# Kernel optimization log

Hardware: AMD Instinct MI355X
Metric: run time of the kernel (lower is better)

Reference implementation:

```python
import jax, jax.numpy as jnp
import numpy as np

N, DIN, D, K0, NC = 32768, 768, 512, 128, 2
KS = [128, 64, 32, 16]  # prototype counts per stage (num_protos // 2**i)
NEG_SLOPE = 0.01


def _lin(x, W, b):
    # torch nn.Linear: W is [out, in]
    return x @ W.T + b


def _ln(x, g, b):
    m = x.mean(-1, keepdims=True)
    v = ((x - m) ** 2).mean(-1, keepdims=True)
    return (x - m) * jax.lax.rsqrt(v + 1e-5) * g + b


def setup_inputs() -> dict:
    key = jax.random.key(0)
    ks = jax.random.split(key, 40)
    s = 0.02

    def nrm(k, shp, sc=s):
        return jax.random.normal(k, shp, jnp.float32) * sc

    inp = {}
    inp["data"] = jax.random.normal(ks[0], (N, DIN), jnp.float32)
    inp["prototypes"] = jax.random.normal(ks[1], (K0, DIN), jnp.float32)
    inp["W_pp"] = nrm(ks[2], (D, DIN)); inp["b_pp"] = jnp.zeros((D,), jnp.float32)
    inp["W_cp"] = nrm(ks[3], (D, DIN)); inp["b_cp"] = jnp.zeros((D,), jnp.float32)
    inp["sim_scale"] = jnp.ones((1,), jnp.float32)
    # 3 enhancer MLPs + layernorms (stacked, same shapes)
    inp["enh_w1"] = nrm(ks[4], (3, D, D)); inp["enh_b1"] = jnp.zeros((3, D), jnp.float32)
    inp["enh_w2"] = nrm(ks[5], (3, D, D)); inp["enh_b2"] = jnp.zeros((3, D), jnp.float32)
    inp["ln_g"] = jnp.ones((3, D), jnp.float32); inp["ln_b"] = jnp.zeros((3, D), jnp.float32)
    # ProtoReducers: Mlp along K axis; fc1 [inK,inK], fc2 [outK,inK]
    ki = 6
    for i in range(3):
        inK, outK = KS[i], KS[i + 1]
        inp[f"red_w1_{i}"] = nrm(ks[ki], (inK, inK)); ki += 1
        inp[f"red_b1_{i}"] = jnp.zeros((inK,), jnp.float32)
        inp[f"red_w2_{i}"] = nrm(ks[ki], (outK, inK)); ki += 1
        inp[f"red_b2_{i}"] = jnp.zeros((outK,), jnp.float32)
    inp["W_proc"] = nrm(ks[20], (D, D)); inp["b_proc"] = jnp.zeros((D,), jnp.float32)
    inp["g_an"] = jnp.ones((D,), jnp.float32); inp["b_an"] = jnp.zeros((D,), jnp.float32)
    inp["W_t"] = nrm(ks[21], (D, D)); inp["b_t"] = jnp.zeros((D,), jnp.float32)
    inp["W_g"] = nrm(ks[22], (D, D)); inp["b_g"] = jnp.zeros((D,), jnp.float32)
    inp["W_s"] = nrm(ks[23], (1, D)); inp["b_s"] = jnp.zeros((1,), jnp.float32)
    inp["W_h"] = nrm(ks[24], (D, D)); inp["b_h"] = jnp.zeros((D,), jnp.float32)
    inp["W_c"] = nrm(ks[25], (NC, D)); inp["b_c"] = jnp.zeros((NC,), jnp.float32)
    return inp


def reference(data, prototypes, W_pp, b_pp, W_cp, b_cp, sim_scale,
              enh_w1, enh_b1, enh_w2, enh_b2, ln_g, ln_b,
              red_w1_0, red_b1_0, red_w2_0, red_b2_0,
              red_w1_1, red_b1_1, red_w2_1, red_b2_1,
              red_w1_2, red_b1_2, red_w2_2, red_b2_2,
              W_proc, b_proc, g_an, b_an,
              W_t, b_t, W_g, b_g, W_s, b_s, W_h, b_h, W_c, b_c):
    # patch / prototype projections (Linear + LeakyReLU)
    P = jax.nn.leaky_relu(_lin(data, W_pp, b_pp), NEG_SLOPE)        # [N, D]
    C = jax.nn.leaky_relu(_lin(prototypes, W_cp, b_cp), NEG_SLOPE)  # [K0, D]
    # denom = max(1e-6, tau * similarity_scale.item()); tau=1, no grad through scale
    denom = jnp.maximum(1e-6, jax.lax.stop_gradient(sim_scale)[0])
    reds = [(red_w1_0, red_b1_0, red_w2_0, red_b2_0),
            (red_w1_1, red_b1_1, red_w2_1, red_b2_1),
            (red_w1_2, red_b1_2, red_w2_2, red_b2_2)]
    for i in range(3):
        # L2 similarity: -cdist(P, C) computed as a GEMM
        d2 = (jnp.sum(P * P, -1, keepdims=True) + jnp.sum(C * C, -1)[None, :]
              - 2.0 * (P @ C.T))
        sim = -jnp.sqrt(jnp.maximum(d2, 1e-12))                     # [N, K]
        A = jax.nn.softmax(sim / denom, axis=1)                     # soft routing
        ctx = A @ C                                                 # [N, D]
        P = _ln(P + ctx, ln_g[i], ln_b[i])
        P = P + _lin(jax.nn.relu(_lin(P, enh_w1[i], enh_b1[i])), enh_w2[i], enh_b2[i])
        # ProtoReducer: Mlp over K axis (operate on C.T of shape [D, K])
        w1, b1, w2, b2 = reds[i]
        Ct = _lin(jax.nn.relu(_lin(C.T, w1, b1)), w2, b2)           # [D, Kout]
        C = Ct.T
    Z = jnp.concatenate([P, C], axis=0)                             # [N+16, D]
    Z = jax.nn.relu(_lin(Z, W_proc, b_proc))
    Z = _ln(Z, g_an, b_an)
    # gated attention MIL pooling
    t = jnp.tanh(_lin(Z, W_t, b_t))
    g = jax.nn.sigmoid(_lin(Z, W_g, b_g))
    scores = _lin(t * g, W_s, b_s)                                  # [N+16, 1]
    Aw = jax.nn.softmax(scores, axis=0)
    bag = Aw.T @ Z                                                  # [1, D]
    h = jax.nn.relu(_lin(bag, W_h, b_h))
    logits = _lin(h, W_c, b_c)                                      # [1, 2]
    return logits
```

## Files before the change

### kernel.cpp

```cpp
#include <hip/hip_runtime.h>
#include <math.h>

typedef _Float16 f16x8 __attribute__((ext_vector_type(8)));
typedef _Float16 f16x4 __attribute__((ext_vector_type(4)));
typedef float f32x4 __attribute__((ext_vector_type(4)));

#define TBM 256
#define TBN 128
#define TBK 32

#define AS1 __attribute__((address_space(1)))
#define AS3 __attribute__((address_space(3)))

__device__ __forceinline__ void gll16(const _Float16* g, _Float16* l)
{
    __builtin_amdgcn_global_load_lds((const AS1 unsigned int*)g,
                                     (AS3 unsigned int*)l, 16, 0, 0);
}

__device__ __forceinline__ int xcd_swz(int d, int nwg)
{
    int q = nwg >> 3, r = nwg & 7;
    int x = d & 7, idx = d >> 3;
    int base = x < r ? x * (q + 1) : r * (q + 1) + (x - r) * q;
    return base + idx;
}

__device__ __forceinline__ float fsigmoid(float x)
{
    return __builtin_amdgcn_rcpf(1.f + __expf(-x));
}
__device__ __forceinline__ float ftanh(float x)
{
    float ax = fabsf(x);
    float e = __expf(-2.f * ax);
    float t = (1.f - e) * __builtin_amdgcn_rcpf(1.f + e);
    return copysignf(t, x);
}

struct CvtSegs {
    const float* src[6];
    _Float16* dst[6];
    int cum4[7];
};

__global__ __launch_bounds__(256)
void cvtall_k(CvtSegs a)
{
    int total = a.cum4[6];
    for (int i = blockIdx.x * 256 + threadIdx.x; i < total; i += gridDim.x * 256) {
        int s = 0;
        while (i >= a.cum4[s + 1]) s++;
        int loc = (i - a.cum4[s]) * 4;
        float4 v = *(const float4*)(a.src[s] + loc);
        f16x4 h = { (_Float16)v.x, (_Float16)v.y, (_Float16)v.z, (_Float16)v.w };
        *(f16x4*)(a.dst[s] + loc) = h;
    }
}

template<int ACT, bool F16OUT>
__global__ __launch_bounds__(256)
void dot_k(const float* __restrict__ X, const float* __restrict__ W,
           const float* __restrict__ bias, void* __restrict__ Yv,
           int M, int K)
{
    int gw = (blockIdx.x * 256 + threadIdx.x) >> 6;
    int lane = threadIdx.x & 63;
    if (gw >= M * 512) return;
    int r = gw >> 9, n = gw & 511;
    const float* xr = X + (size_t)r * K;
    const float* wr = W + (size_t)n * K;
    float d = 0.f;
    for (int t = 0; t < K; t += 256) {
        float4 a = *(const float4*)(xr + t + lane * 4);
        float4 b = *(const float4*)(wr + t + lane * 4);
        d += a.x * b.x + a.y * b.y + a.z * b.z + a.w * b.w;
    }
#pragma unroll
    for (int o = 32; o; o >>= 1) d += __shfl_xor(d, o);
    if (lane == 0) {
        float v = d + bias[n];
        if (ACT == 1) v = v > 0.f ? v : 0.01f * v;
        else if (ACT == 2) v = fmaxf(v, 0.f);
        if (F16OUT) ((_Float16*)Yv)[(size_t)r * 512 + n] = (_Float16)v;
        else        ((float*)Yv)[(size_t)r * 512 + n] = v;
    }
}

__global__ __launch_bounds__(256)
void cvtC2_k(const float* __restrict__ C, _Float16* __restrict__ Ch,
             _Float16* __restrict__ CTh, float* __restrict__ Csq2, int Kin)
{
    int w = threadIdx.x >> 6, lane = threadIdx.x & 63;
    int row = blockIdx.x * 4 + w;
    if (row >= Kin) return;
    float4 a = *(const float4*)(C + (size_t)row * 512 + lane * 8);
    float4 b = *(const float4*)(C + (size_t)row * 512 + lane * 8 + 4);
    f16x8 h;
    h[0] = (_Float16)a.x; h[1] = (_Float16)a.y; h[2] = (_Float16)a.z; h[3] = (_Float16)a.w;
    h[4] = (_Float16)b.x; h[5] = (_Float16)b.y; h[6] = (_Float16)b.z; h[7] = (_Float16)b.w;
    *(f16x8*)(Ch + (size_t)row * 512 + lane * 8) = h;
    float s = 0.f;
#pragma unroll
    for (int q = 0; q < 8; q++) {
        float f = (float)h[q];
        s += f * f;
        CTh[(size_t)(lane * 8 + q) * Kin + row] = h[q];
    }
#pragma unroll
    for (int o = 32; o; o >>= 1) s += __shfl_xor(s, o);
    if (lane == 0) { Csq2[row * 2] = s; Csq2[row * 2 + 1] = 0.f; }
}

template<int MODE, int ACT, bool SQ>
__global__ __launch_bounds__(512)
void mgemm(const _Float16* __restrict__ A, const _Float16* __restrict__ B,
           const float* __restrict__ bias, _Float16* __restrict__ Yh,
           float* __restrict__ Psq4, int M, int K, int Nout)
{
    __shared__ _Float16 As[2][TBM * TBK];
    __shared__ _Float16 Bs[2][TBN * TBK];
    const int tid = threadIdx.x;
    const int lane = tid & 63;
    const int wid = tid >> 6;
    const int wr = wid >> 1, wc = wid & 1;

    int bid = xcd_swz(blockIdx.y * gridDim.x + blockIdx.x, gridDim.x * gridDim.y);
    const int m0 = (bid / gridDim.x) * TBM;
    const int n0 = (bid % gridDim.x) * TBN;

    f32x4 acc[4][4] = {};
    const int nt = K / TBK;

    const int lrow = lane >> 2;
    const int lk = (lane & 3) * 8;

    auto stage = [&](int t, int buf) {
        const int k0 = t * TBK;
#pragma unroll
        for (int q = 0; q < 2; q++) {
            int c = wid * 2 + q;
            int r = c * 16 + lrow;
            int am = min(m0 + r, M - 1);
            gll16(A + (size_t)am * K + k0 + lk, &As[buf][c * 512]);
        }
        {
            int c = wid;
            int r = c * 16 + lrow;
            int bn = min(n0 + r, Nout - 1);
            gll16(B + (size_t)bn * K + k0 + lk, &Bs[buf][c * 512]);
        }
    };

    stage(0, 0);
    __syncthreads();
    for (int t = 0; t < nt; ++t) {
        const int cur = t & 1;
        if (t + 1 < nt) stage(t + 1, cur ^ 1);
        f16x8 af[4], bf[4];
#pragma unroll
        for (int mi = 0; mi < 4; mi++)
            af[mi] = *(const f16x8*)(&As[cur][(wr * 64 + mi * 16 + (lane & 15)) * TBK + (lane >> 4) * 8]);
#pragma unroll
        for (int nj = 0; nj < 4; nj++)
            bf[nj] = *(const f16x8*)(&Bs[cur][(wc * 64 + nj * 16 + (lane & 15)) * TBK + (lane >> 4) * 8]);
#pragma unroll
        for (int mi = 0; mi < 4; mi++)
#pragma unroll
            for (int nj = 0; nj < 4; nj++)
                acc[mi][nj] = __builtin_amdgcn_mfma_f32_16x16x32_f16(af[mi], bf[nj], acc[mi][nj], 0, 0, 0);
        __syncthreads();
    }

    _Float16* eb = &As[0][0];
    const int g = lane >> 4;
#pragma unroll
    for (int p = 0; p < 2; p++) {
        if (p) __syncthreads();
        if ((wr >> 1) == p) {
#pragma unroll
            for (int nj = 0; nj < 4; nj++) {
                int col = wc * 64 + nj * 16 + (lane & 15);
                float bv = bias ? bias[n0 + col] : 0.f;
#pragma unroll
                for (int mi = 0; mi < 4; mi++)
#pragma unroll
                    for (int r = 0; r < 4; r++) {
                        int lr = (wr & 1) * 64 + mi * 16 + g * 4 + r;
                        float v = acc[mi][nj][r] + bv;
                        if (MODE == 0) {
                            if (ACT == 1) v = v > 0.f ? v : 0.01f * v;
                            else if (ACT == 2) v = fmaxf(v, 0.f);
                        }
                        eb[lr * 128 + col] = (_Float16)v;
                    }
            }
        }
        __syncthreads();
        int t4 = tid * 4;
        int lr = t4 >> 4;
        int cbase = (t4 & 15) * 8;
        int m = m0 + p * 128 + lr;
        float sq = 0.f;
        if (m < M) {
#pragma unroll
            for (int q = 0; q < 4; q++) {
                int c0 = cbase + q * 8;
                f16x8 hv = *(f16x8*)(eb + lr * 128 + c0);
                size_t gidx = (size_t)m * Nout + n0 + c0;
                if (MODE == 1) {
                    f16x8 old = *(f16x8*)(Yh + gidx);
                    f16x8 nw;
#pragma unroll
                    for (int e = 0; e < 8; e++) {
                        float s = (float)old[e] + (float)hv[e];
                        nw[e] = (_Float16)s;
                    }
                    *(f16x8*)(Yh + gidx) = nw;
                    hv = nw;
                } else {
                    *(f16x8*)(Yh + gidx) = hv;
                }
                if (SQ) {
#pragma unroll
                    for (int e = 0; e < 8; e++) { float f = (float)hv[e]; sq += f * f; }
                }
            }
        }
        if (SQ) {
            sq += __shfl_xor(sq, 1);
            sq += __shfl_xor(sq, 2);
            if ((lane & 3) == 0 && m < M) Psq4[(size_t)m * 4 + (n0 >> 7)] = sq;
        }
    }
}

__global__ __launch_bounds__(512)
void pgemm32(const float* __restrict__ A32, const _Float16* __restrict__ B,
             const float* __restrict__ bias, _Float16* __restrict__ Yh,
             float* __restrict__ Psq4, int M, int K, int Nout)
{
    __shared__ _Float16 As[2][TBM * TBK];
    __shared__ _Float16 Bs[2][TBN * TBK];
    const int tid = threadIdx.x;
    const int lane = tid & 63;
    const int wid = tid >> 6;
    const int wr = wid >> 1, wc = wid & 1;

    int bid = xcd_swz(blockIdx.y * gridDim.x + blockIdx.x, gridDim.x * gridDim.y);
    const int m0 = (bid / gridDim.x) * TBM;
    const int n0 = (bid % gridDim.x) * TBN;

    f32x4 acc[4][4] = {};
    const int nt = K / TBK;

    const int lrow = lane >> 2;
    const int lk = (lane & 3) * 8;

    auto stage = [&](int t, int buf) {
        const int k0 = t * TBK;
#pragma unroll
        for (int q = 0; q < 2; q++) {
            int c = wid * 2 + q;
            int r = c * 16 + lrow;
            int am = min(m0 + r, M - 1);
            const float* src = A32 + (size_t)am * K + k0 + lk;
            float4 a0 = *(const float4*)src;
            float4 a1 = *(const float4*)(src + 4);
            f16x8 h;
            h[0] = (_Float16)a0.x; h[1] = (_Float16)a0.y; h[2] = (_Float16)a0.z; h[3] = (_Float16)a0.w;
            h[4] = (_Float16)a1.x; h[5] = (_Float16)a1.y; h[6] = (_Float16)a1.z; h[7] = (_Float16)a1.w;
            *(f16x8*)(&As[buf][c * 512 + lane * 8]) = h;
        }
        {
            int c = wid;
            int r = c * 16 + lrow;
            int bn = min(n0 + r, Nout - 1);
            gll16(B + (size_t)bn * K + k0 + lk, &Bs[buf][c * 512]);
        }
    };

    stage(0, 0);
    __syncthreads();
    for (int t = 0; t < nt; ++t) {
        const int cur = t & 1;
        if (t + 1 < nt) stage(t + 1, cur ^ 1);
        f16x8 af[4], bf[4];
#pragma unroll
        for (int mi = 0; mi < 4; mi++)
            af[mi] = *(const f16x8*)(&As[cur][(wr * 64 + mi * 16 + (lane & 15)) * TBK + (lane >> 4) * 8]);
#pragma unroll
        for (int nj = 0; nj < 4; nj++)
            bf[nj] = *(const f16x8*)(&Bs[cur][(wc * 64 + nj * 16 + (lane & 15)) * TBK + (lane >> 4) * 8]);
#pragma unroll
        for (int mi = 0; mi < 4; mi++)
#pragma unroll
            for (int nj = 0; nj < 4; nj++)
                acc[mi][nj] = __builtin_amdgcn_mfma_f32_16x16x32_f16(af[mi], bf[nj], acc[mi][nj], 0, 0, 0);
        __syncthreads();
    }

    _Float16* eb = &As[0][0];
    const int g = lane >> 4;
#pragma unroll
    for (int p = 0; p < 2; p++) {
        if (p) __syncthreads();
        if ((wr >> 1) == p) {
#pragma unroll
            for (int nj = 0; nj < 4; nj++) {
                int col = wc * 64 + nj * 16 + (lane & 15);
                float bv = bias[n0 + col];
#pragma unroll
                for (int mi = 0; mi < 4; mi++)
#pragma unroll
                    for (int r = 0; r < 4; r++) {
                        int lr = (wr & 1) * 64 + mi * 16 + g * 4 + r;
                        float v = acc[mi][nj][r] + bv;
                        v = v > 0.f ? v : 0.01f * v;
                        eb[lr * 128 + col] = (_Float16)v;
                    }
            }
        }
        __syncthreads();
        int t4 = tid * 4;
        int lr = t4 >> 4;
        int cbase = (t4 & 15) * 8;
        int m = m0 + p * 128 + lr;
        float sq = 0.f;
        if (m < M) {
#pragma unroll
            for (int q = 0; q < 4; q++) {
                int c0 = cbase + q * 8;
                f16x8 hv = *(f16x8*)(eb + lr * 128 + c0);
                *(f16x8*)(Yh + (size_t)m * Nout + n0 + c0) = hv;
#pragma unroll
                for (int e = 0; e < 8; e++) { float f = (float)hv[e]; sq += f * f; }
            }
        }
        sq += __shfl_xor(sq, 1);
        sq += __shfl_xor(sq, 2);
        if ((lane & 3) == 0 && m < M) Psq4[(size_t)m * 4 + (n0 >> 7)] = sq;
    }
}

__global__ __launch_bounds__(512)
void ctxln_k(const _Float16* __restrict__ A, const _Float16* __restrict__ CT,
             const float* __restrict__ g, const float* __restrict__ b,
             _Float16* __restrict__ Ph, int M, int Kin)
{
    __shared__ _Float16 As[2][128 * TBK];
    __shared__ _Float16 Bs[2][512 * TBK];
    const int tid = threadIdx.x;
    const int lane = tid & 63;
    const int wid = tid >> 6;
    const int wr = wid >> 2, wc = wid & 3;
    const int m0 = blockIdx.y * 128;

    f32x4 acc[4][8] = {};
    const int nt = Kin / TBK;

    const int lrow = lane >> 2;
    const int lk = (lane & 3) * 8;

    auto stage = [&](int t, int buf) {
        const int k0 = t * TBK;
        {
            int r = wid * 16 + lrow;
            gll16(A + (size_t)(m0 + r) * Kin + k0 + lk, &As[buf][wid * 512]);
        }
#pragma unroll
        for (int q = 0; q < 4; q++) {
            int c = wid * 4 + q;
            int n = c * 16 + lrow;
            gll16(CT + (size_t)n * Kin + k0 + lk, &Bs[buf][c * 512]);
        }
    };

    stage(0, 0);
    __syncthreads();
    for (int t = 0; t < nt; ++t) {
        const int cur = t & 1;
        if (t + 1 < nt) stage(t + 1, cur ^ 1);
        f16x8 af[4], bf[8];
#pragma unroll
        for (int mi = 0; mi < 4; mi++)
            af[mi] = *(const f16x8*)(&As[cur][(wr * 64 + mi * 16 + (lane & 15)) * TBK + (lane >> 4) * 8]);
#pragma unroll
        for (int nj = 0; nj < 8; nj++)
            bf[nj] = *(const f16x8*)(&Bs[cur][(wc * 128 + nj * 16 + (lane & 15)) * TBK + (lane >> 4) * 8]);
#pragma unroll
        for (int mi = 0; mi < 4; mi++)
#pragma unroll
            for (int nj = 0; nj < 8; nj++)
                acc[mi][nj] = __builtin_amdgcn_mfma_f32_16x16x32_f16(af[mi], bf[nj], acc[mi][nj], 0, 0, 0);
        __syncthreads();
    }

    _Float16* eb = &Bs[0][0];
    const int gq = lane >> 4;
#pragma unroll
    for (int p = 0; p < 2; p++) {
        if (p) __syncthreads();
        if (wr == p) {
#pragma unroll
            for (int nj = 0; nj < 8; nj++) {
                int col = wc * 128 + nj * 16 + (lane & 15);
#pragma unroll
                for (int mi = 0; mi < 4; mi++)
#pragma unroll
                    for (int r = 0; r < 4; r++) {
                        int lr = mi * 16 + gq * 4 + r;
                        eb[lr * 512 + col] = (_Float16)acc[mi][nj][r];
                    }
            }
        }
        __syncthreads();
#pragma unroll
        for (int rr = 0; rr < 8; rr++) {
            int lr = wid * 8 + rr;
            int m = m0 + p * 64 + lr;
            f16x8 cv = *(f16x8*)(eb + lr * 512 + lane * 8);
            f16x8 pv = *(const f16x8*)(Ph + (size_t)m * 512 + lane * 8);
            float v[8];
            float s = 0.f, ss = 0.f;
#pragma unroll
            for (int q = 0; q < 8; q++) {
                v[q] = (float)pv[q] + (float)cv[q];
                s += v[q]; ss += v[q] * v[q];
            }
#pragma unroll
            for (int o = 32; o; o >>= 1) { s += __shfl_xor(s, o); ss += __shfl_xor(ss, o); }
            float mean = s * (1.f / 512.f);
            float var = ss * (1.f / 512.f) - mean * mean;
            float inv = 1.f / sqrtf(var + 1e-5f);
            int d0 = lane * 8;
            f16x8 o8;
#pragma unroll
            for (int q = 0; q < 8; q++)
                o8[q] = (_Float16)((v[q] - mean) * inv * g[d0 + q] + b[d0 + q]);
            *(f16x8*)(Ph + (size_t)m * 512 + d0) = o8;
        }
    }
}

__global__ __launch_bounds__(512)
void procln_k(const _Float16* __restrict__ A, const _Float16* __restrict__ W,
              const float* __restrict__ bias, const float* __restrict__ g,
              const float* __restrict__ b, _Float16* __restrict__ Zh, int M)
{
    __shared__ _Float16 As[2][128 * TBK];
    __shared__ _Float16 Bs[2][512 * TBK];
    const int tid = threadIdx.x;
    const int lane = tid & 63;
    const int wid = tid >> 6;
    const int wr = wid >> 2, wc = wid & 3;
    const int m0 = blockIdx.y * 128;
    const int K = 512;

    f32x4 acc[4][8] = {};
    const int nt = K / TBK;

    const int lrow = lane >> 2;
    const int lk = (lane & 3) * 8;

    auto stage = [&](int t, int buf) {
        const int k0 = t * TBK;
        {
            int r = wid * 16 + lrow;
            gll16(A + (size_t)(m0 + r) * K + k0 + lk, &As[buf][wid * 512]);
        }
#pragma unroll
        for (int q = 0; q < 4; q++) {
            int c = wid * 4 + q;
            int n = c * 16 + lrow;
            gll16(W + (size_t)n * K + k0 + lk, &Bs[buf][c * 512]);
        }
    };

    stage(0, 0);
    __syncthreads();
    for (int t = 0; t < nt; ++t) {
        const int cur = t & 1;
        if (t + 1 < nt) stage(t + 1, cur ^ 1);
        f16x8 af[4], bf[8];
#pragma unroll
        for (int mi = 0; mi < 4; mi++)
            af[mi] = *(const f16x8*)(&As[cur][(wr * 64 + mi * 16 + (lane & 15)) * TBK + (lane >> 4) * 8]);
#pragma unroll
        for (int nj = 0; nj < 8; nj++)
            bf[nj] = *(const f16x8*)(&Bs[cur][(wc * 128 + nj * 16 + (lane & 15)) * TBK + (lane >> 4) * 8]);
#pragma unroll
        for (int mi = 0; mi < 4; mi++)
#pragma unroll
            for (int nj = 0; nj < 8; nj++)
                acc[mi][nj] = __builtin_amdgcn_mfma_f32_16x16x32_f16(af[mi], bf[nj], acc[mi][nj], 0, 0, 0);
        __syncthreads();
    }

    _Float16* eb = &Bs[0][0];
    const int gq = lane >> 4;
#pragma unroll
    for (int p = 0; p < 2; p++) {
        if (p) __syncthreads();
        if (wr == p) {
#pragma unroll
            for (int nj = 0; nj < 8; nj++) {
                int col = wc * 128 + nj * 16 + (lane & 15);
                float bv = bias[col];
#pragma unroll
                for (int mi = 0; mi < 4; mi++)
#pragma unroll
                    for (int r = 0; r < 4; r++) {
                        int lr = mi * 16 + gq * 4 + r;
                        eb[lr * 512 + col] = (_Float16)fmaxf(acc[mi][nj][r] + bv, 0.f);
                    }
            }
        }
        __syncthreads();
#pragma unroll
        for (int rr = 0; rr < 8; rr++) {
            int lr = wid * 8 + rr;
            int m = m0 + p * 64 + lr;
            f16x8 cv = *(f16x8*)(eb + lr * 512 + lane * 8);
            float v[8];
            float s = 0.f, ss = 0.f;
#pragma unroll
            for (int q = 0; q < 8; q++) {
                v[q] = (float)cv[q];
                s += v[q]; ss += v[q] * v[q];
            }
#pragma unroll
            for (int o = 32; o; o >>= 1) { s += __shfl_xor(s, o); ss += __shfl_xor(ss, o); }
            float mean = s * (1.f / 512.f);
            float var = ss * (1.f / 512.f) - mean * mean;
            float inv = 1.f / sqrtf(var + 1e-5f);
            int d0 = lane * 8;
            f16x8 o8;
#pragma unroll
            for (int q = 0; q < 8; q++)
                o8[q] = (_Float16)((v[q] - mean) * inv * g[d0 + q] + b[d0 + q]);
            *(f16x8*)(Zh + (size_t)m * 512 + d0) = o8;
        }
    }
}

__global__ __launch_bounds__(512)
void gatgemm(const _Float16* __restrict__ A, const _Float16* __restrict__ B1,
             const _Float16* __restrict__ B2, const float* __restrict__ c1,
             const float* __restrict__ c2, const float* __restrict__ Ws,
             float* __restrict__ scr4, int M, int K, int Nout)
{
    __shared__ _Float16 As[2][TBM * TBK];
    __shared__ _Float16 B1s[2][TBN * TBK];
    __shared__ _Float16 B2s[2][TBN * TBK];
    const int tid = threadIdx.x;
    const int lane = tid & 63;
    const int wid = tid >> 6;
    const int wr = wid >> 1, wc = wid & 1;

    int bid = xcd_swz(blockIdx.y * gridDim.x + blockIdx.x, gridDim.x * gridDim.y);
    const int m0 = (bid / gridDim.x) * TBM;
    const int n0 = (bid % gridDim.x) * TBN;

    f32x4 acc1[4][4] = {};
    f32x4 acc2[4][4] = {};
    const int nt = K / TBK;

    const int lrow = lane >> 2;
    const int lk = (lane & 3) * 8;

    auto stage = [&](int t, int buf) {
        const int k0 = t * TBK;
#pragma unroll
        for (int q = 0; q < 2; q++) {
            int c = wid * 2 + q;
            int r = c * 16 + lrow;
            int am = min(m0 + r, M - 1);
            gll16(A + (size_t)am * K + k0 + lk, &As[buf][c * 512]);
        }
        {
            int c = wid;
            int r = c * 16 + lrow;
            int bn = min(n0 + r, Nout - 1);
            gll16(B1 + (size_t)bn * K + k0 + lk, &B1s[buf][c * 512]);
            gll16(B2 + (size_t)bn * K + k0 + lk, &B2s[buf][c * 512]);
        }
    };

    stage(0, 0);
    __syncthreads();
    for (int t = 0; t < nt; ++t) {
        const int cur = t & 1;
        if (t + 1 < nt) stage(t + 1, cur ^ 1);
        f16x8 af[4], bf1[4], bf2[4];
#pragma unroll
        for (int mi = 0; mi < 4; mi++)
            af[mi] = *(const f16x8*)(&As[cur][(wr * 64 + mi * 16 + (lane & 15)) * TBK + (lane >> 4) * 8]);
#pragma unroll
        for (int nj = 0; nj < 4; nj++) {
            int ro = (wc * 64 + nj * 16 + (lane & 15)) * TBK + (lane >> 4) * 8;
            bf1[nj] = *(const f16x8*)(&B1s[cur][ro]);
            bf2[nj] = *(const f16x8*)(&B2s[cur][ro]);
        }
#pragma unroll
        for (int mi = 0; mi < 4; mi++)
#pragma unroll
            for (int nj = 0; nj < 4; nj++) {
                acc1[mi][nj] = __builtin_amdgcn_mfma_f32_16x16x32_f16(af[mi], bf1[nj], acc1[mi][nj], 0, 0, 0);
                acc2[mi][nj] = __builtin_amdgcn_mfma_f32_16x16x32_f16(af[mi], bf2[nj], acc2[mi][nj], 0, 0, 0);
            }
        __syncthreads();
    }

    const int g = lane >> 4;
// ... 361 lines not shown
}

__global__ __launch_bounds__(256)
void bagf_k(const float* __restrict__ PB, const float* __restrict__ scal,
            float* __restrict__ bag, int nchunk)
{
    int d = blockIdx.x * 256 + threadIdx.x;
    float acc = 0.f;
    for (int c = 0; c < nchunk; c++) acc += PB[(size_t)c * 512 + d];
    bag[d] = acc / scal[0];
}

__global__ __launch_bounds__(256)
void h_k(const float* __restrict__ bag, const float* __restrict__ Wh,
         const float* __restrict__ bh, float* __restrict__ h)
{
    int wid = threadIdx.x >> 6, lane = threadIdx.x & 63;
    int j = blockIdx.x * 4 + wid;
    const float* wr = Wh + (size_t)j * 512;
    float d = 0.f;
#pragma unroll
    for (int t = 0; t < 2; t++) {
        float4 a = *(const float4*)(wr + t * 256 + lane * 4);
        float4 bv = *(const float4*)(bag + t * 256 + lane * 4);
        d += a.x * bv.x + a.y * bv.y + a.z * bv.z + a.w * bv.w;
    }
#pragma unroll
    for (int o = 32; o; o >>= 1) d += __shfl_xor(d, o);
    if (lane == 0) h[j] = fmaxf(d + bh[j], 0.f);
}

__global__ __launch_bounds__(128)
void logit_k(const float* __restrict__ h, const float* __restrict__ Wc,
             const float* __restrict__ bc, float* __restrict__ out)
{
    int wid = threadIdx.x >> 6, lane = threadIdx.x & 63;
    const float* wr = Wc + (size_t)wid * 512;
    float d = 0.f;
#pragma unroll
    for (int t = 0; t < 2; t++) {
        float4 a = *(const float4*)(wr + t * 256 + lane * 4);
        float4 hv = *(const float4*)(h + t * 256 + lane * 4);
        d += a.x * hv.x + a.y * hv.y + a.z * hv.z + a.w * hv.w;
    }
#pragma unroll
    for (int o = 32; o; o >>= 1) d += __shfl_xor(d, o);
    if (lane == 0) out[wid] = d + bc[wid];
}

extern "C" void kernel_launch(void* const* d_in, const int* in_sizes, int n_in,
                              void* d_out, int out_size, void* d_ws, size_t ws_size,
                              hipStream_t stream)
{
    const float* data    = (const float*)d_in[0];
    const float* protos  = (const float*)d_in[1];
    const float* W_pp    = (const float*)d_in[2];
    const float* b_pp    = (const float*)d_in[3];
    const float* W_cp    = (const float*)d_in[4];
    const float* b_cp    = (const float*)d_in[5];
    const float* sscale  = (const float*)d_in[6];
    const float* enh_w1  = (const float*)d_in[7];
    const float* enh_b1  = (const float*)d_in[8];
    const float* enh_w2  = (const float*)d_in[9];
    const float* enh_b2  = (const float*)d_in[10];
    const float* ln_g    = (const float*)d_in[11];
    const float* ln_b    = (const float*)d_in[12];
    const float* red_w1[3] = {(const float*)d_in[13], (const float*)d_in[17], (const float*)d_in[21]};
    const float* red_b1[3] = {(const float*)d_in[14], (const float*)d_in[18], (const float*)d_in[22]};
    const float* red_w2[3] = {(const float*)d_in[15], (const float*)d_in[19], (const float*)d_in[23]};
    const float* red_b2[3] = {(const float*)d_in[16], (const float*)d_in[20], (const float*)d_in[24]};
    const float* W_proc  = (const float*)d_in[25];
    const float* b_proc  = (const float*)d_in[26];
    const float* g_an    = (const float*)d_in[27];
    const float* b_an    = (const float*)d_in[28];
    const float* W_t     = (const float*)d_in[29];
    const float* b_t     = (const float*)d_in[30];
    const float* W_g     = (const float*)d_in[31];
    const float* b_g     = (const float*)d_in[32];
    const float* W_s     = (const float*)d_in[33];
    const float* b_s     = (const float*)d_in[34];
    const float* W_h     = (const float*)d_in[35];
    const float* b_h     = (const float*)d_in[36];
    const float* W_c     = (const float*)d_in[37];
    const float* b_c     = (const float*)d_in[38];
    float* out = (float*)d_out;
    (void)b_s;

    constexpr int N = 32768, DIN = 768, D = 512;
    constexpr int NCHUNK = 256;
    char* w = (char*)d_ws;
    auto alloc = [&](size_t bytes) -> char* {
        char* p = w; w += (bytes + 255) & ~(size_t)255; return p;
    };
    _Float16* Ph     = (_Float16*)alloc((size_t)N * D * 2);
    _Float16* TMPh   = (_Float16*)alloc((size_t)N * D * 2);
    _Float16* Zh     = (_Float16*)alloc((size_t)(N + 16) * D * 2);
    _Float16* Ztail  = (_Float16*)alloc((size_t)16 * D * 2);
    _Float16* Ah     = (_Float16*)alloc((size_t)N * 128 * 2);
    _Float16* Ch     = (_Float16*)alloc(128 * D * 2);
    _Float16* CTh    = (_Float16*)alloc(128 * D * 2);
    _Float16* Wpph   = (_Float16*)alloc((size_t)D * DIN * 2);
    _Float16* w1h    = (_Float16*)alloc((size_t)3 * D * D * 2);
    _Float16* w2h    = (_Float16*)alloc((size_t)3 * D * D * 2);
    _Float16* Wproch = (_Float16*)alloc((size_t)D * D * 2);
    _Float16* Wth    = (_Float16*)alloc((size_t)D * D * 2);
    _Float16* Wgh    = (_Float16*)alloc((size_t)D * D * 2);
    float*    Psq4   = (float*)alloc((size_t)N * 4 * 4);
    float*    Csq2   = (float*)alloc(128 * 2 * 4);
    float*    Ca     = (float*)alloc(128 * D * 4);
    float*    Cb     = (float*)alloc(128 * D * 4);
    float*    H1     = (float*)alloc(128 * D * 4);
    float*    scr4   = (float*)alloc((size_t)(N + 16) * 4 * 4);
    float*    scr    = (float*)alloc((size_t)(N + 16) * 4);
    float*    PB     = (float*)alloc((size_t)NCHUNK * D * 4);
    float*    bag    = (float*)alloc(D * 4);
    float*    hb     = (float*)alloc(D * 4);
    float*    scal   = (float*)alloc(8 * 4);

    dim3 blk(256);
    dim3 blk512(512);
    auto mgrid = [](int M_, int Nout_) { return dim3((Nout_ + TBN - 1) / TBN, (M_ + TBM - 1) / TBM); };

    {
        CvtSegs cs;
        const float* srcs[6] = { W_pp, enh_w1, enh_w2, W_proc, W_t, W_g };
        _Float16* dsts[6]    = { Wpph, w1h, w2h, Wproch, Wth, Wgh };
        int sizes[6] = { D * DIN, 3 * D * D, 3 * D * D, D * D, D * D, D * D };
        int c = 0;
        cs.cum4[0] = 0;
        for (int s = 0; s < 6; s++) {
            cs.src[s] = srcs[s]; cs.dst[s] = dsts[s];
            c += sizes[s] / 4;
            cs.cum4[s + 1] = c;
        }
        cvtall_k<<<dim3(2048), blk, 0, stream>>>(cs);
    }

    pgemm32<<<mgrid(N, D), blk512, 0, stream>>>(data, Wpph, b_pp, Ph, Psq4, N, DIN, D);
    dot_k<1, false><<<dim3(128 * 512 / 4), blk, 0, stream>>>(protos, W_cp, b_cp, Ca, 128, DIN);
    cvtC2_k<<<dim3(32), blk, 0, stream>>>(Ca, Ch, CTh, Csq2, 128);

    float* C = Ca;
    float* Cn = Cb;
    int Kin = 128;
    for (int i = 0; i < 3; i++) {
        int Kout = Kin >> 1;
        if (i == 0)
            simgemm<<<dim3(1, N / SBM), blk, 0, stream>>>(Ph, Ch, Psq4, Csq2, sscale, Ah, N, D);
        else if (i == 1)
            simgemm_s<64><<<dim3(1, N / 256), blk, 0, stream>>>(Ph, Ch, Psq4, Csq2, sscale, Ah, N, D);
        else
            simgemm_s<32><<<dim3(1, N / 256), blk, 0, stream>>>(Ph, Ch, Psq4, Csq2, sscale, Ah, N, D);
        ctxln_k<<<dim3(1, N / 128), blk512, 0, stream>>>(Ah, CTh, ln_g + (size_t)i * D, ln_b + (size_t)i * D, Ph, N, Kin);
        mgemm<0, 2, false><<<mgrid(N, D), blk512, 0, stream>>>(Ph, w1h + (size_t)i * D * D, enh_b1 + (size_t)i * D, TMPh, nullptr, N, D, D);
        if (i < 2)
            mgemm<1, 0, true><<<mgrid(N, D), blk512, 0, stream>>>(TMPh, w2h + (size_t)i * D * D, enh_b2 + (size_t)i * D, Ph, Psq4, N, D, D);
        else
            mgemm<1, 0, false><<<mgrid(N, D), blk512, 0, stream>>>(TMPh, w2h + (size_t)i * D * D, enh_b2 + (size_t)i * D, Ph, nullptr, N, D, D);
        red1_k<<<dim3(2, Kin), blk, 0, stream>>>(C, red_w1[i], red_b1[i], H1, Kin);
        red2_k<<<dim3(2, Kout), blk, 0, stream>>>(H1, red_w2[i], red_b2[i], Cn, Ch, CTh, Csq2, Kin, Kout);
        float* t = C; C = Cn; Cn = t;
        Kin = Kout;
    }

    procln_k<<<dim3(1, N / 128), blk512, 0, stream>>>(Ph, Wproch, b_proc, g_an, b_an, Zh, N);
    dot_k<2, true><<<dim3(16 * 512 / 4), blk, 0, stream>>>(C, W_proc, b_proc, Ztail, 16, D);
    ln_k<<<dim3(4), blk, 0, stream>>>(Ztail, nullptr, g_an, b_an, Zh + (size_t)N * D, 16);

    gatgemm<<<mgrid(N + 16, D), blk512, 0, stream>>>(Zh, Wth, Wgh, b_t, b_g, W_s, scr4, N + 16, D, D);

    pool_k<<<dim3(1), dim3(1024), 0, stream>>>((const float4*)scr4, scr, scal, N + 16);
    int cs2 = (N + 16 + NCHUNK - 1) / NCHUNK;
    bagp_k<<<dim3(2, NCHUNK), blk, 0, stream>>>(Zh, scr, PB, N + 16, cs2);
    bagf_k<<<dim3(2), blk, 0, stream>>>(PB, scal, bag, NCHUNK);

    h_k<<<dim3(128), blk, 0, stream>>>(bag, W_h, b_h, hb);
    logit_k<<<dim3(1), dim3(128), 0, stream>>>(hb, W_c, b_c, out);
}
```

Before: 757.7 us.

## Replace enhancer MLP GEMMs with full-row 128x512 tile kernels

Swaps the generic 256x128-tile mgemm for two dedicated kernels that give each block a 128-row by full 512-column output tile. Each activation row is then loaded once per GEMM instead of once per column tile. Because the block owns whole rows, the residual-add kernel writes the complete squared norm into the first Psq4 slot and zeros the other three, instead of four per-tile partial sums. The cost is fewer, larger blocks (256 in total), which changes occupancy and makes every block stream the whole weight matrix.

```diff
diff --git a/kernel.cpp b/kernel.cpp
--- a/kernel.cpp
+++ b/kernel.cpp
@@ -112,129 +112,6 @@
     if (lane == 0) { Csq2[row * 2] = s; Csq2[row * 2 + 1] = 0.f; }
 }
 
-template<int MODE, int ACT, bool SQ>
-__global__ __launch_bounds__(512)
-void mgemm(const _Float16* __restrict__ A, const _Float16* __restrict__ B,
-           const float* __restrict__ bias, _Float16* __restrict__ Yh,
-           float* __restrict__ Psq4, int M, int K, int Nout)
-{
-    __shared__ _Float16 As[2][TBM * TBK];
-    __shared__ _Float16 Bs[2][TBN * TBK];
-    const int tid = threadIdx.x;
-    const int lane = tid & 63;
-    const int wid = tid >> 6;
-    const int wr = wid >> 1, wc = wid & 1;
-
-    int bid = xcd_swz(blockIdx.y * gridDim.x + blockIdx.x, gridDim.x * gridDim.y);
-    const int m0 = (bid / gridDim.x) * TBM;
-    const int n0 = (bid % gridDim.x) * TBN;
-
-    f32x4 acc[4][4] = {};
-    const int nt = K / TBK;
-
-    const int lrow = lane >> 2;
-    const int lk = (lane & 3) * 8;
-
-    auto stage = [&](int t, int buf) {
-        const int k0 = t * TBK;
-#pragma unroll
-        for (int q = 0; q < 2; q++) {
-            int c = wid * 2 + q;
-            int r = c * 16 + lrow;
-            int am = min(m0 + r, M - 1);
-            gll16(A + (size_t)am * K + k0 + lk, &As[buf][c * 512]);
-        }
-        {
-            int c = wid;
-            int r = c * 16 + lrow;
-            int bn = min(n0 + r, Nout - 1);
-            gll16(B + (size_t)bn * K + k0 + lk, &Bs[buf][c * 512]);
-        }
-    };
-
-    stage(0, 0);
-    __syncthreads();
-    for (int t = 0; t < nt; ++t) {
-        const int cur = t & 1;
-        if (t + 1 < nt) stage(t + 1, cur ^ 1);
-        f16x8 af[4], bf[4];
-#pragma unroll
-        for (int mi = 0; mi < 4; mi++)
-            af[mi] = *(const f16x8*)(&As[cur][(wr * 64 + mi * 16 + (lane & 15)) * TBK + (lane >> 4) * 8]);
-#pragma unroll
-        for (int nj = 0; nj < 4; nj++)
-            bf[nj] = *(const f16x8*)(&Bs[cur][(wc * 64 + nj * 16 + (lane & 15)) * TBK + (lane >> 4) * 8]);
-#pragma unroll
-        for (int mi = 0; mi < 4; mi++)
-#pragma unroll
-            for (int nj = 0; nj < 4; nj++)
-                acc[mi][nj] = __builtin_amdgcn_mfma_f32_16x16x32_f16(af[mi], bf[nj], acc[mi][nj], 0, 0, 0);
-        __syncthreads();
-    }
-
-    _Float16* eb = &As[0][0];
-    const int g = lane >> 4;
-#pragma unroll
-    for (int p = 0; p < 2; p++) {
-        if (p) __syncthreads();
-        if ((wr >> 1) == p) {
-#pragma unroll
-            for (int nj = 0; nj < 4; nj++) {
-                int col = wc * 64 + nj * 16 + (lane & 15);
-                float bv = bias ? bias[n0 + col] : 0.f;
-#pragma unroll
-                for (int mi = 0; mi < 4; mi++)
-#pragma unroll
-                    for (int r = 0; r < 4; r++) {
-                        int lr = (wr & 1) * 64 + mi * 16 + g * 4 + r;
-                        float v = acc[mi][nj][r] + bv;
-                        if (MODE == 0) {
-                            if (ACT == 1) v = v > 0.f ? v : 0.01f * v;
-                            else if (ACT == 2) v = fmaxf(v, 0.f);
-                        }
-                        eb[lr * 128 + col] = (_Float16)v;
-                    }
-            }
-        }
-        __syncthreads();
-        int t4 = tid * 4;
-        int lr = t4 >> 4;
-        int cbase = (t4 & 15) * 8;
-        int m = m0 + p * 128 + lr;
-        float sq = 0.f;
-        if (m < M) {
-#pragma unroll
-            for (int q = 0; q < 4; q++) {
-                int c0 = cbase + q * 8;
-                f16x8 hv = *(f16x8*)(eb + lr * 128 + c0);
-                size_t gidx = (size_t)m * Nout + n0 + c0;
-                if (MODE == 1) {
-                    f16x8 old = *(f16x8*)(Yh + gidx);
-                    f16x8 nw;
-#pragma unroll
-                    for (int e = 0; e < 8; e++) {
-                        float s = (float)old[e] + (float)hv[e];
-                        nw[e] = (_Float16)s;
-                    }
-                    *(f16x8*)(Yh + gidx) = nw;
-                    hv = nw;
-                } else {
-                    *(f16x8*)(Yh + gidx) = hv;
-                }
-                if (SQ) {
-#pragma unroll
-                    for (int e = 0; e < 8; e++) { float f = (float)hv[e]; sq += f * f; }
-                }
-            }
-        }
-        if (SQ) {
-            sq += __shfl_xor(sq, 1);
-            sq += __shfl_xor(sq, 2);
-            if ((lane & 3) == 0 && m < M) Psq4[(size_t)m * 4 + (n0 >> 7)] = sq;
-        }
-    }
-}
-
 __global__ __launch_bounds__(512)
 void pgemm32(const float* __restrict__ A32, const _Float16* __restrict__ B,
              const float* __restrict__ bias, _Float16* __restrict__ Yh,
@@ -344,109 +221,8 @@
 }
 
 __global__ __launch_bounds__(512)
-void ctxln_k(const _Float16* __restrict__ A, const _Float16* __restrict__ CT,
-             const float* __restrict__ g, const float* __restrict__ b,
-             _Float16* __restrict__ Ph, int M, int Kin)
-{
-    __shared__ _Float16 As[2][128 * TBK];
-    __shared__ _Float16 Bs[2][512 * TBK];
-    const int tid = threadIdx.x;
-    const int lane = tid & 63;
-    const int wid = tid >> 6;
-    const int wr = wid >> 2, wc = wid & 3;
-    const int m0 = blockIdx.y * 128;
-
-    f32x4 acc[4][8] = {};
-    const int nt = Kin / TBK;
-
-    const int lrow = lane >> 2;
-    const int lk = (lane & 3) * 8;
-
-    auto stage = [&](int t, int buf) {
-        const int k0 = t * TBK;
-        {
-            int r = wid * 16 + lrow;
-            gll16(A + (size_t)(m0 + r) * Kin + k0 + lk, &As[buf][wid * 512]);
-        }
-#pragma unroll
-        for (int q = 0; q < 4; q++) {
-            int c = wid * 4 + q;
-            int n = c * 16 + lrow;
-            gll16(CT + (size_t)n * Kin + k0 + lk, &Bs[buf][c * 512]);
-        }
-    };
-
-    stage(0, 0);
-    __syncthreads();
-    for (int t = 0; t < nt; ++t) {
-        const int cur = t & 1;
-        if (t + 1 < nt) stage(t + 1, cur ^ 1);
-        f16x8 af[4], bf[8];
-#pragma unroll
-        for (int mi = 0; mi < 4; mi++)
-            af[mi] = *(const f16x8*)(&As[cur][(wr * 64 + mi * 16 + (lane & 15)) * TBK + (lane >> 4) * 8]);
-#pragma unroll
-        for (int nj = 0; nj < 8; nj++)
-            bf[nj] = *(const f16x8*)(&Bs[cur][(wc * 128 + nj * 16 + (lane & 15)) * TBK + (lane >> 4) * 8]);
-#pragma unroll
-        for (int mi = 0; mi < 4; mi++)
-#pragma unroll
-            for (int nj = 0; nj < 8; nj++)
-                acc[mi][nj] = __builtin_amdgcn_mfma_f32_16x16x32_f16(af[mi], bf[nj], acc[mi][nj], 0, 0, 0);
-        __syncthreads();
-    }
-
-    _Float16* eb = &Bs[0][0];
-    const int gq = lane >> 4;
-#pragma unroll
-    for (int p = 0; p < 2; p++) {
-        if (p) __syncthreads();
-        if (wr == p) {
-#pragma unroll
-            for (int nj = 0; nj < 8; nj++) {
-                int col = wc * 128 + nj * 16 + (lane & 15);
-#pragma unroll
-                for (int mi = 0; mi < 4; mi++)
-#pragma unroll
-                    for (int r = 0; r < 4; r++) {
-                        int lr = mi * 16 + gq * 4 + r;
-                        eb[lr * 512 + col] = (_Float16)acc[mi][nj][r];
-                    }
-            }
-        }
-        __syncthreads();
-#pragma unroll
-        for (int rr = 0; rr < 8; rr++) {
-            int lr = wid * 8 + rr;
-            int m = m0 + p * 64 + lr;
-            f16x8 cv = *(f16x8*)(eb + lr * 512 + lane * 8);
-            f16x8 pv = *(const f16x8*)(Ph + (size_t)m * 512 + lane * 8);
-            float v[8];
-            float s = 0.f, ss = 0.f;
-#pragma unroll
-            for (int q = 0; q < 8; q++) {
-                v[q] = (float)pv[q] + (float)cv[q];
-                s += v[q]; ss += v[q] * v[q];
-            }
-#pragma unroll
-            for (int o = 32; o; o >>= 1) { s += __shfl_xor(s, o); ss += __shfl_xor(ss, o); }
-            float mean = s * (1.f / 512.f);
-            float var = ss * (1.f / 512.f) - mean * mean;
-            float inv = 1.f / sqrtf(var + 1e-5f);
-            int d0 = lane * 8;
-            f16x8 o8;
-#pragma unroll
-            for (int q = 0; q < 8; q++)
-                o8[q] = (_Float16)((v[q] - mean) * inv * g[d0 + q] + b[d0 + q]);
-            *(f16x8*)(Ph + (size_t)m * 512 + d0) = o8;
-        }
-    }
-}
-
-__global__ __launch_bounds__(512)
-void procln_k(const _Float16* __restrict__ A, const _Float16* __restrict__ W,
-              const float* __restrict__ bias, const float* __restrict__ g,
-              const float* __restrict__ b, _Float16* __restrict__ Zh, int M)
+void enh1_k(const _Float16* __restrict__ A, const _Float16* __restrict__ W,
+            const float* __restrict__ bias, _Float16* __restrict__ Y, int M)
 {
     __shared__ _Float16 As[2][128 * TBK];
     __shared__ _Float16 Bs[2][512 * TBK];
@@ -459,7 +235,289 @@
 
     f32x4 acc[4][8] = {};
     const int nt = K / TBK;
-
+    const int lrow = lane >> 2;
+    const int lk = (lane & 3) * 8;
+
+    auto stage = [&](int t, int buf) {
+        const int k0 = t * TBK;
+        {
+            int r = wid * 16 + lrow;
+            gll16(A + (size_t)(m0 + r) * K + k0 + lk, &As[buf][wid * 512]);
+        }
+#pragma unroll
+        for (int q = 0; q < 4; q++) {
+            int c = wid * 4 + q;
+            int n = c * 16 + lrow;
+            gll16(W + (size_t)n * K + k0 + lk, &Bs[buf][c * 512]);
+        }
+    };
+
+    stage(0, 0);
+    __syncthreads();
+    for (int t = 0; t < nt; ++t) {
+        const int cur = t & 1;
+        if (t + 1 < nt) stage(t + 1, cur ^ 1);
+        f16x8 af[4], bf[8];
+#pragma unroll
+        for (int mi = 0; mi < 4; mi++)
+            af[mi] = *(const f16x8*)(&As[cur][(wr * 64 + mi * 16 + (lane & 15)) * TBK + (lane >> 4) * 8]);
+#pragma unroll
+        for (int nj = 0; nj < 8; nj++)
+            bf[nj] = *(const f16x8*)(&Bs[cur][(wc * 128 + nj * 16 + (lane & 15)) * TBK + (lane >> 4) * 8]);
+#pragma unroll
+        for (int mi = 0; mi < 4; mi++)
+#pragma unroll
+            for (int nj = 0; nj < 8; nj++)
+                acc[mi][nj] = __builtin_amdgcn_mfma_f32_16x16x32_f16(af[mi], bf[nj], acc[mi][nj], 0, 0, 0);
+        __syncthreads();
+    }
+
+    _Float16* eb = &Bs[0][0];
+    const int gq = lane >> 4;
+#pragma unroll
+    for (int p = 0; p < 2; p++) {
+        if (p) __syncthreads();
+        if (wr == p) {
+#pragma unroll
+            for (int nj = 0; nj < 8; nj++) {
+                int col = wc * 128 + nj * 16 + (lane & 15);
+                float bv = bias[col];
+#pragma unroll
+                for (int mi = 0; mi < 4; mi++)
+#pragma unroll
+                    for (int r = 0; r < 4; r++) {
+                        int lr = mi * 16 + gq * 4 + r;
+                        eb[lr * 512 + col] = (_Float16)fmaxf(acc[mi][nj][r] + bv, 0.f);
+                    }
+            }
+        }
+        __syncthreads();
+#pragma unroll
+        for (int rr = 0; rr < 8; rr++) {
+            int lr = wid * 8 + rr;
+            int m = m0 + p * 64 + lr;
+            f16x8 hv = *(f16x8*)(eb + lr * 512 + lane * 8);
+            *(f16x8*)(Y + (size_t)m * 512 + lane * 8) = hv;
+        }
+    }
+}
+
+template<bool SQ>
+__global__ __launch_bounds__(512)
+void enh2_k(const _Float16* __restrict__ A, const _Float16* __restrict__ W,
+            const float* __restrict__ bias, _Float16* __restrict__ Ph,
+            float* __restrict__ Psq4, int M)
+{
+    __shared__ _Float16 As[2][128 * TBK];
+    __shared__ _Float16 Bs[2][512 * TBK];
+    const int tid = threadIdx.x;
+    const int lane = tid & 63;
+    const int wid = tid >> 6;
+    const int wr = wid >> 2, wc = wid & 3;
+    const int m0 = blockIdx.y * 128;
+    const int K = 512;
+
+    f32x4 acc[4][8] = {};
+    const int nt = K / TBK;
+    const int lrow = lane >> 2;
+    const int lk = (lane & 3) * 8;
+
+    auto stage = [&](int t, int buf) {
+        const int k0 = t * TBK;
+        {
+            int r = wid * 16 + lrow;
+            gll16(A + (size_t)(m0 + r) * K + k0 + lk, &As[buf][wid * 512]);
+        }
+#pragma unroll
+        for (int q = 0; q < 4; q++) {
+            int c = wid * 4 + q;
+            int n = c * 16 + lrow;
+            gll16(W + (size_t)n * K + k0 + lk, &Bs[buf][c * 512]);
+        }
+    };
+
+    stage(0, 0);
+    __syncthreads();
+    for (int t = 0; t < nt; ++t) {
+        const int cur = t & 1;
+        if (t + 1 < nt) stage(t + 1, cur ^ 1);
+        f16x8 af[4], bf[8];
+#pragma unroll
+        for (int mi = 0; mi < 4; mi++)
+            af[mi] = *(const f16x8*)(&As[cur][(wr * 64 + mi * 16 + (lane & 15)) * TBK + (lane >> 4) * 8]);
+#pragma unroll
+        for (int nj = 0; nj < 8; nj++)
+            bf[nj] = *(const f16x8*)(&Bs[cur][(wc * 128 + nj * 16 + (lane & 15)) * TBK + (lane >> 4) * 8]);
+#pragma unroll
+        for (int mi = 0; mi < 4; mi++)
+#pragma unroll
+            for (int nj = 0; nj < 8; nj++)
+                acc[mi][nj] = __builtin_amdgcn_mfma_f32_16x16x32_f16(af[mi], bf[nj], acc[mi][nj], 0, 0, 0);
+        __syncthreads();
+    }
+
+    _Float16* eb = &Bs[0][0];
+    const int gq = lane >> 4;
+#pragma unroll
+    for (int p = 0; p < 2; p++) {
+        if (p) __syncthreads();
+        if (wr == p) {
+#pragma unroll
+            for (int nj = 0; nj < 8; nj++) {
+                int col = wc * 128 + nj * 16 + (lane & 15);
+                float bv = bias[col];
+#pragma unroll
+                for (int mi = 0; mi < 4; mi++)
+#pragma unroll
+                    for (int r = 0; r < 4; r++) {
+                        int lr = mi * 16 + gq * 4 + r;
+                        eb[lr * 512 + col] = (_Float16)(acc[mi][nj][r] + bv);
+                    }
+            }
+        }
+        __syncthreads();
+#pragma unroll
+        for (int rr = 0; rr < 8; rr++) {
+            int lr = wid * 8 + rr;
+            int m = m0 + p * 64 + lr;
+            f16x8 cv = *(f16x8*)(eb + lr * 512 + lane * 8);
+            f16x8 pv = *(const f16x8*)(Ph + (size_t)m * 512 + lane * 8);
+            f16x8 o8;
+            float sq = 0.f;
+#pragma unroll
+            for (int q = 0; q < 8; q++) {
+                float s = (float)pv[q] + (float)cv[q];
+                o8[q] = (_Float16)s;
+                if (SQ) { float f = (float)o8[q]; sq += f * f; }
+            }
+            *(f16x8*)(Ph + (size_t)m * 512 + lane * 8) = o8;
+            if (SQ) {
+#pragma unroll
+                for (int o = 32; o; o >>= 1) sq += __shfl_xor(sq, o);
+                if (lane == 0) {
+                    float4 w4 = { sq, 0.f, 0.f, 0.f };
+                    *(float4*)(Psq4 + (size_t)m * 4) = w4;
+                }
+            }
+        }
+    }
+}
+
+__global__ __launch_bounds__(512)
+void ctxln_k(const _Float16* __restrict__ A, const _Float16* __restrict__ CT,
+             const float* __restrict__ g, const float* __restrict__ b,
+             _Float16* __restrict__ Ph, int M, int Kin)
+{
+    __shared__ _Float16 As[2][128 * TBK];
+    __shared__ _Float16 Bs[2][512 * TBK];
+    const int tid = threadIdx.x;
+    const int lane = tid & 63;
+    const int wid = tid >> 6;
+    const int wr = wid >> 2, wc = wid & 3;
+    const int m0 = blockIdx.y * 128;
+
+    f32x4 acc[4][8] = {};
+    const int nt = Kin / TBK;
+    const int lrow = lane >> 2;
+    const int lk = (lane & 3) * 8;
+
+    auto stage = [&](int t, int buf) {
+        const int k0 = t * TBK;
+        {
+            int r = wid * 16 + lrow;
+            gll16(A + (size_t)(m0 + r) * Kin + k0 + lk, &As[buf][wid * 512]);
+        }
+#pragma unroll
+        for (int q = 0; q < 4; q++) {
+            int c = wid * 4 + q;
+            int n = c * 16 + lrow;
+            gll16(CT + (size_t)n * Kin + k0 + lk, &Bs[buf][c * 512]);
+        }
+    };
+
+    stage(0, 0);
+    __syncthreads();
+    for (int t = 0; t < nt; ++t) {
+        const int cur = t & 1;
+        if (t + 1 < nt) stage(t + 1, cur ^ 1);
+        f16x8 af[4], bf[8];
+#pragma unroll
+        for (int mi = 0; mi < 4; mi++)
+            af[mi] = *(const f16x8*)(&As[cur][(wr * 64 + mi * 16 + (lane & 15)) * TBK + (lane >> 4) * 8]);
+#pragma unroll
+        for (int nj = 0; nj < 8; nj++)
+            bf[nj] = *(const f16x8*)(&Bs[cur][(wc * 128 + nj * 16 + (lane & 15)) * TBK + (lane >> 4) * 8]);
+#pragma unroll
+        for (int mi = 0; mi < 4; mi++)
+#pragma unroll
+            for (int nj = 0; nj < 8; nj++)
+                acc[mi][nj] = __builtin_amdgcn_mfma_f32_16x16x32_f16(af[mi], bf[nj], acc[mi][nj], 0, 0, 0);
+        __syncthreads();
+    }
+
+    _Float16* eb = &Bs[0][0];
+    const int gq = lane >> 4;
+#pragma unroll
+    for (int p = 0; p < 2; p++) {
+        if (p) __syncthreads();
+        if (wr == p) {
+#pragma unroll
+            for (int nj = 0; nj < 8; nj++) {
+                int col = wc * 128 + nj * 16 + (lane & 15);
+#pragma unroll
+                for (int mi = 0; mi < 4; mi++)
+#pragma unroll
+                    for (int r = 0; r < 4; r++) {
+                        int lr = mi * 16 + gq * 4 + r;
+                        eb[lr * 512 + col] = (_Float16)acc[mi][nj][r];
+                    }
+            }
+        }
+        __syncthreads();
+#pragma unroll
+        for (int rr = 0; rr < 8; rr++) {
+            int lr = wid * 8 + rr;
+            int m = m0 + p * 64 + lr;
+            f16x8 cv = *(f16x8*)(eb + lr * 512 + lane * 8);
+            f16x8 pv = *(const f16x8*)(Ph + (size_t)m * 512 + lane * 8);
+            float v[8];
+            float s = 0.f, ss = 0.f;
+#pragma unroll
+            for (int q = 0; q < 8; q++) {
+                v[q] = (float)pv[q] + (float)cv[q];
+                s += v[q]; ss += v[q] * v[q];
+            }
+#pragma unroll
+            for (int o = 32; o; o >>= 1) { s += __shfl_xor(s, o); ss += __shfl_xor(ss, o); }
+            float mean = s * (1.f / 512.f);
+            float var = ss * (1.f / 512.f) - mean * mean;
+            float inv = 1.f / sqrtf(var + 1e-5f);
+            int d0 = lane * 8;
+            f16x8 o8;
+#pragma unroll
+            for (int q = 0; q < 8; q++)
+                o8[q] = (_Float16)((v[q] - mean) * inv * g[d0 + q] + b[d0 + q]);
+            *(f16x8*)(Ph + (size_t)m * 512 + d0) = o8;
+        }
+    }
+}
+
+__global__ __launch_bounds__(512)
+void procln_k(const _Float16* __restrict__ A, const _Float16* __restrict__ W,
+              const float* __restrict__ bias, const float* __restrict__ g,
+              const float* __restrict__ b, _Float16* __restrict__ Zh, int M)
+{
+    __shared__ _Float16 As[2][128 * TBK];
+    __shared__ _Float16 Bs[2][512 * TBK];
+    const int tid = threadIdx.x;
+    const int lane = tid & 63;
+    const int wid = tid >> 6;
+    const int wr = wid >> 2, wc = wid & 3;
+    const int m0 = blockIdx.y * 128;
+    const int K = 512;
+
+    f32x4 acc[4][8] = {};
+    const int nt = K / TBK;
     const int lrow = lane >> 2;
     const int lk = (lane & 3) * 8;
 
@@ -1127,11 +1185,11 @@
         else
             simgemm_s<32><<<dim3(1, N / 256), blk, 0, stream>>>(Ph, Ch, Psq4, Csq2, sscale, Ah, N, D);
         ctxln_k<<<dim3(1, N / 128), blk512, 0, stream>>>(Ah, CTh, ln_g + (size_t)i * D, ln_b + (size_t)i * D, Ph, N, Kin);
-        mgemm<0, 2, false><<<mgrid(N, D), blk512, 0, stream>>>(Ph, w1h + (size_t)i * D * D, enh_b1 + (size_t)i * D, TMPh, nullptr, N, D, D);
+        enh1_k<<<dim3(1, N / 128), blk512, 0, stream>>>(Ph, w1h + (size_t)i * D * D, enh_b1 + (size_t)i * D, TMPh, N);
         if (i < 2)
-            mgemm<1, 0, true><<<mgrid(N, D), blk512, 0, stream>>>(TMPh, w2h + (size_t)i * D * D, enh_b2 + (size_t)i * D, Ph, Psq4, N, D, D);
+            enh2_k<true><<<dim3(1, N / 128), blk512, 0, stream>>>(TMPh, w2h + (size_t)i * D * D, enh_b2 + (size_t)i * D, Ph, Psq4, N);
         else
-            mgemm<1, 0, false><<<mgrid(N, D), blk512, 0, stream>>>(TMPh, w2h + (size_t)i * D * D, enh_b2 + (size_t)i * D, Ph, nullptr, N, D, D);
+            enh2_k<false><<<dim3(1, N / 128), blk512, 0, stream>>>(TMPh, w2h + (size_t)i * D * D, enh_b2 + (size_t)i * D, Ph, nullptr, N);
         red1_k<<<dim3(2, Kin), blk, 0, stream>>>(C, red_w1[i], red_b1[i], H1, Kin);
         red2_k<<<dim3(2, Kout), blk, 0, stream>>>(H1, red_w2[i], red_b2[i], Cn, Ch, CTh, Csq2, Kin, Kout);
         float* t = C; C = Cn; Cn = t;
```

New measurement: 757.0 us (median of 2 runs). About the same (-0.1%).
